# Optimization experiments

Measured on AMD Instinct MI355X. Metric: run time of the kernel, lower is better.

The kernel has to match this reference:

```python
import jax, jax.numpy as jnp
import numpy as np

B, I, H = 16384, 512, 512


def setup_inputs() -> dict:
    key = jax.random.key(0)
    ks = jax.random.split(key, 6)
    scale_s = 1.0 / np.sqrt(H + I + 1)
    scale_g = 1.0 / np.sqrt(H + I + H)
    return {
        "x_t": jax.random.normal(ks[0], (B, I), dtype=jnp.float32),
        "delta_t": jax.random.uniform(ks[1], (B, 1), dtype=jnp.float32),
        "h_prev": jax.random.normal(ks[2], (B, H), dtype=jnp.float32),
        "c_prev": jax.random.normal(ks[3], (B, H), dtype=jnp.float32),
        # linear_s: in = H + I + 1
        "Ws": jax.random.normal(ks[4], (H + I + 1, H), dtype=jnp.float32) * scale_s,
        "bs": jnp.zeros((H,), dtype=jnp.float32),
        # stacked weights for the 5 gates (f, i, T, u, o), each in = H + I + H
        "Wg": jax.random.normal(ks[5], (2 * H + I, 5 * H), dtype=jnp.float32) * scale_g,
        "bg": jnp.zeros((5 * H,), dtype=jnp.float32),
    }


def reference(x_t, delta_t, h_prev, c_prev, Ws, bs, Wg, bg):
    # time gate: s_t = tanh(Linear([h_prev, x_t, delta_t]))
    s_t = jnp.tanh(jnp.concatenate([h_prev, x_t, delta_t], axis=1) @ Ws + bs)
    # shared-input GEMM for the 5 gates on concat([h_prev, x_t, s_t])
    z = jnp.concatenate([h_prev, x_t, s_t], axis=1) @ Wg + bg  # [B, 5H]
    f_t = jax.nn.sigmoid(z[:, 0 * H:1 * H])
    i_t = jax.nn.sigmoid(z[:, 1 * H:2 * H])
    T_t = jax.nn.sigmoid(z[:, 2 * H:3 * H])
    zeta_t = jnp.tanh(z[:, 3 * H:4 * H])
    o_t = jax.nn.sigmoid(z[:, 4 * H:5 * H])
    c_t = f_t * c_prev + i_t * zeta_t + T_t * s_t
    h_t = o_t * jnp.tanh(c_t)
    return (h_t, c_t)
```

## Files before the change

kernel.cpp:

```cpp
#include <hip/hip_runtime.h>
#include <stdint.h>
#include <stddef.h>

#define Bsz 16384
#define Hsz 512
#define KG 1536
#define KA 1024

typedef float f32x4 __attribute__((ext_vector_type(4)));
typedef short bf16x8 __attribute__((ext_vector_type(8)));
typedef unsigned short u16;

__device__ __forceinline__ u16 f2bf(float f) {
  union { float f; unsigned u; } v; v.f = f;
  return (u16)((v.u + 0x7fffu + ((v.u >> 16) & 1u)) >> 16);
}
__device__ __forceinline__ float bf2f(u16 h) {
  union { unsigned u; float f; } v; v.u = ((unsigned)h) << 16;
  return v.f;
}
__device__ __forceinline__ float sigm(float x) {
  return 1.0f / (1.0f + __expf(-x));
}
__device__ __forceinline__ float tanh_(float x) {
  x = fminf(fmaxf(x, -15.0f), 15.0f);
  float e = __expf(2.0f * x);
  return (e - 1.0f) / (e + 1.0f);
}

__device__ __forceinline__ void gload_lds16(const u16* g, u16* l) {
  __builtin_amdgcn_global_load_lds(
      (__attribute__((address_space(1))) void*)(g),
      (__attribute__((address_space(3))) void*)(l), 16, 0, 0);
}

__global__ __launch_bounds__(256) void prep_A_kernel(
    const float* __restrict__ h_prev, const float* __restrict__ x_t,
    u16* __restrict__ A) {
  const int b = blockIdx.x;
  const int q = threadIdx.x;
  const int qq = q & 127;
  const float4* src = (q < 128) ? (const float4*)h_prev : (const float4*)x_t;
  float4 v = src[(size_t)b * 128 + qq];
  ushort4 o;
  o.x = f2bf(v.x); o.y = f2bf(v.y); o.z = f2bf(v.z); o.w = f2bf(v.w);
  *(ushort4*)(A + (size_t)b * KG + (size_t)q * 4) = o;
}

__global__ __launch_bounds__(256) void transpose_cast_kernel(
    const float* __restrict__ in, u16* __restrict__ out, int R, int C) {
  __shared__ float tile[32][33];
  const int c0 = blockIdx.x * 32;
  const int r0 = blockIdx.y * 32;
  const int tx = threadIdx.x;
  const int ty = threadIdx.y;
  #pragma unroll
  for (int i = ty; i < 32; i += 8)
    tile[i][tx] = in[(size_t)(r0 + i) * C + (c0 + tx)];
  __syncthreads();
  #pragma unroll
  for (int i = ty; i < 32; i += 8)
    out[(size_t)(c0 + i) * R + (r0 + tx)] = f2bf(tile[tx][i]);
}

__global__ __launch_bounds__(256, 2) void gemm1_kernel(
    const u16* __restrict__ A, const u16* __restrict__ Wst,
    const float* __restrict__ Ws, const float* __restrict__ bs,
    const float* __restrict__ delta, u16* __restrict__ Aout) {
  __shared__ __attribute__((aligned(16))) u16 Als[128][32];
  __shared__ __attribute__((aligned(16))) u16 Bls[128][32];
  const int t = threadIdx.x;
  const int w = t >> 6, l = t & 63;
  const int bm0 = blockIdx.y * 128;
  const int bn0 = blockIdx.x * 128;
  const int wm = w >> 1, wn = w & 1;

  f32x4 zv = {0.f, 0.f, 0.f, 0.f};
  f32x4 acc[4][4];
  #pragma unroll
  for (int i = 0; i < 4; ++i)
    #pragma unroll
    for (int j = 0; j < 4; ++j) acc[i][j] = zv;

  const int r = t >> 2, q = t & 3;
  const u16* gA0 = A + (size_t)(bm0 + r) * KG + q * 8;
  const u16* gA1 = A + (size_t)(bm0 + 64 + r) * KG + q * 8;
  const u16* gB0 = Wst + (size_t)(bn0 + r) * KA + q * 8;
  const u16* gB1 = Wst + (size_t)(bn0 + 64 + r) * KA + q * 8;
  u16* lA0 = &Als[0][0] + w * 512;
  u16* lA1 = &Als[0][0] + 2048 + w * 512;
  u16* lB0 = &Bls[0][0] + w * 512;
  u16* lB1 = &Bls[0][0] + 2048 + w * 512;

  const int frow = l & 15;
  const int kofs = (l >> 4) * 8;

  for (int kt = 0; kt < KA / 32; ++kt) {
    const int ko = kt * 32;
    gload_lds16(gA0 + ko, lA0);
    gload_lds16(gA1 + ko, lA1);
    gload_lds16(gB0 + ko, lB0);
    gload_lds16(gB1 + ko, lB1);
    __syncthreads();
    bf16x8 af[4], bfv[4];
    #pragma unroll
    for (int mi = 0; mi < 4; ++mi)
      af[mi] = *(const bf16x8*)&Als[wm * 64 + mi * 16 + frow][kofs];
    #pragma unroll
    for (int ni = 0; ni < 4; ++ni)
      bfv[ni] = *(const bf16x8*)&Bls[wn * 64 + ni * 16 + frow][kofs];
    #pragma unroll
    for (int mi = 0; mi < 4; ++mi)
      #pragma unroll
      for (int ni = 0; ni < 4; ++ni)
        acc[mi][ni] = __builtin_amdgcn_mfma_f32_16x16x32_bf16(
            af[mi], bfv[ni], acc[mi][ni], 0, 0, 0);
    __syncthreads();
  }

  #pragma unroll
  for (int ni = 0; ni < 4; ++ni) {
    const int col = bn0 + wn * 64 + ni * 16 + (l & 15);
    const float wsl = Ws[(size_t)1024 * 512 + col];
    const float bsv = bs[col];
    #pragma unroll
    for (int mi = 0; mi < 4; ++mi) {
      #pragma unroll
      for (int rr = 0; rr < 4; ++rr) {
        const int row = bm0 + wm * 64 + mi * 16 + (l >> 4) * 4 + rr;
        const float z = acc[mi][ni][rr] + delta[row] * wsl + bsv;
        Aout[(size_t)row * KG + 1024 + col] = f2bf(tanh_(z));
      }
    }
  }
}

__global__ __launch_bounds__(256, 2) void gemm2_kernel(
    const u16* __restrict__ A, const u16* __restrict__ Wgt,
    const float* __restrict__ bg, const float* __restrict__ c_prev,
    float* __restrict__ out) {
  __shared__ __attribute__((aligned(16))) u16 Als[128][32];
  __shared__ __attribute__((aligned(16))) u16 Bls[160][32];
  const int t = threadIdx.x;
  const int w = t >> 6, l = t & 63;
  const int bm0 = blockIdx.y * 128;
  const int h0 = blockIdx.x * 32;
  const int wm = w >> 1, wh = w & 1;

  f32x4 zv = {0.f, 0.f, 0.f, 0.f};
  f32x4 acc[4][5];
  #pragma unroll
  for (int i = 0; i < 4; ++i)
    #pragma unroll
    for (int j = 0; j < 5; ++j) acc[i][j] = zv;

  const int r = t >> 2, q = t & 3;
  const u16* gA0 = A + (size_t)(bm0 + r) * KG + q * 8;
  const u16* gA1 = A + (size_t)(bm0 + 64 + r) * KG + q * 8;
  const u16* gB0 = Wgt + (size_t)(((r) >> 5) * Hsz + h0 + ((r) & 31)) * KG + q * 8;
  const u16* gB1 = Wgt + (size_t)(((r + 64) >> 5) * Hsz + h0 + ((r + 64) & 31)) * KG + q * 8;
  const u16* gB2 = Wgt + (size_t)(((r + 128) >> 5) * Hsz + h0 + ((r + 128) & 31)) * KG + q * 8;
  u16* lA0 = &Als[0][0] + w * 512;
  u16* lA1 = &Als[0][0] + 2048 + w * 512;
  u16* lB0 = &Bls[0][0] + w * 512;
  u16* lB1 = &Bls[0][0] + 2048 + w * 512;
  u16* lB2 = &Bls[0][0] + 4096 + w * 512;

  const int frow = l & 15;
  const int kofs = (l >> 4) * 8;

  for (int kt = 0; kt < KG / 32; ++kt) {
    const int ko = kt * 32;
    gload_lds16(gA0 + ko, lA0);
    gload_lds16(gA1 + ko, lA1);
    gload_lds16(gB0 + ko, lB0);
    gload_lds16(gB1 + ko, lB1);
    if (t < 128) gload_lds16(gB2 + ko, lB2);
    __syncthreads();
    bf16x8 af[4], bfv[5];
    #pragma unroll
    for (int mi = 0; mi < 4; ++mi)
      af[mi] = *(const bf16x8*)&Als[wm * 64 + mi * 16 + frow][kofs];
    #pragma unroll
    for (int g = 0; g < 5; ++g)
      bfv[g] = *(const bf16x8*)&Bls[g * 32 + wh * 16 + frow][kofs];
    #pragma unroll
    for (int mi = 0; mi < 4; ++mi)
      #pragma unroll
      for (int g = 0; g < 5; ++g)
        acc[mi][g] = __builtin_amdgcn_mfma_f32_16x16x32_bf16(
            af[mi], bfv[g], acc[mi][g], 0, 0, 0);
    __syncthreads();
  }

  const int hc = h0 + wh * 16 + (l & 15);
  const float b_f = bg[hc];
  const float b_i = bg[Hsz + hc];
  const float b_T = bg[2 * Hsz + hc];
  const float b_z = bg[3 * Hsz + hc];
  const float b_o = bg[4 * Hsz + hc];
  #pragma unroll
  for (int mi = 0; mi < 4; ++mi) {
    #pragma unroll
    for (int rr = 0; rr < 4; ++rr) {
      const int row = bm0 + wm * 64 + mi * 16 + (l >> 4) * 4 + rr;
      const float fg = sigm(acc[mi][0][rr] + b_f);
      const float ig = sigm(acc[mi][1][rr] + b_i);
      const float Tg = sigm(acc[mi][2][rr] + b_T);
      const float zg = tanh_(acc[mi][3][rr] + b_z);
      const float og = sigm(acc[mi][4][rr] + b_o);
      const float cp = c_prev[(size_t)row * Hsz + hc];
      const float st = bf2f(A[(size_t)row * KG + 1024 + hc]);
      const float c = fg * cp + ig * zg + Tg * st;
      const float h = og * tanh_(c);
      out[(size_t)row * Hsz + hc] = h;
      out[(size_t)Bsz * Hsz + (size_t)row * Hsz + hc] = c;
    }
  }
}

extern "C" void kernel_launch(void* const* d_in, const int* in_sizes, int n_in,
                              void* d_out, int out_size, void* d_ws, size_t ws_size,
                              hipStream_t stream) {
  const float* x_t    = (const float*)d_in[0];
  const float* delta  = (const float*)d_in[1];
  const float* h_prev = (const float*)d_in[2];
  const float* c_prev = (const float*)d_in[3];
  const float* Ws     = (const float*)d_in[4];
  const float* bs     = (const float*)d_in[5];
  const float* Wg     = (const float*)d_in[6];
  const float* bg     = (const float*)d_in[7];
  float* out = (float*)d_out;

  char* wsb = (char*)d_ws;
  u16* A   = (u16*)(wsb);
  u16* Wst = (u16*)(wsb + (size_t)50331648);
  u16* Wgt = (u16*)(wsb + (size_t)51380224);

  prep_A_kernel<<<dim3(16384), dim3(256), 0, stream>>>(h_prev, x_t, A);
  transpose_cast_kernel<<<dim3(16, 32), dim3(32, 8), 0, stream>>>(Ws, Wst, 1024, 512);
  transpose_cast_kernel<<<dim3(80, 48), dim3(32, 8), 0, stream>>>(Wg, Wgt, 1536, 2560);
  gemm1_kernel<<<dim3(4, 128), dim3(256), 0, stream>>>(A, Wst, Ws, bs, delta, A);
  gemm2_kernel<<<dim3(16, 128), dim3(256), 0, stream>>>(A, Wgt, bg, c_prev, out);
}
```

Before: 220.1 us.

## Rewrite gate GEMM with 4-stage async LDS pipeline, larger tiles and swizzle

The gate GEMM kernel is replaced by a 512-thread version that computes 256x(5*64) tiles. It uses a 4-deep ring of LDS buffers filled by global_load_lds, with explicit vmcnt waits so loads run three K-steps ahead of compute. A XOR swizzle on the LDS layout reduces bank conflicts, and s_setprio is raised around the MFMA block. The aim is to hide global-load latency and improve data reuse. The cost is higher LDS use (about 144KB per block) and more accumulator registers, which may limit occupancy.

```diff
diff --git a/kernel.cpp b/kernel.cpp
--- a/kernel.cpp
+++ b/kernel.cpp
@@ -6,10 +6,12 @@
 #define Hsz 512
 #define KG 1536
 #define KA 1024
+#define NT 48
 
 typedef float f32x4 __attribute__((ext_vector_type(4)));
 typedef short bf16x8 __attribute__((ext_vector_type(8)));
 typedef unsigned short u16;
+typedef unsigned int u32;
 
 __device__ __forceinline__ u16 f2bf(float f) {
   union { float f; unsigned u; } v; v.f = f;
@@ -33,6 +35,8 @@
       (__attribute__((address_space(1))) void*)(g),
       (__attribute__((address_space(3))) void*)(l), 16, 0, 0);
 }
+
+#define VMCNT(n) asm volatile("s_waitcnt vmcnt(" #n ")" ::: "memory")
 
 __global__ __launch_bounds__(256) void prep_A_kernel(
     const float* __restrict__ h_prev, const float* __restrict__ x_t,
@@ -135,75 +139,122 @@
   }
 }
 
-__global__ __launch_bounds__(256, 2) void gemm2_kernel(
+__global__ __launch_bounds__(512, 2) void gemm2_8ph(
     const u16* __restrict__ A, const u16* __restrict__ Wgt,
     const float* __restrict__ bg, const float* __restrict__ c_prev,
     float* __restrict__ out) {
-  __shared__ __attribute__((aligned(16))) u16 Als[128][32];
-  __shared__ __attribute__((aligned(16))) u16 Bls[160][32];
-  const int t = threadIdx.x;
-  const int w = t >> 6, l = t & 63;
-  const int bm0 = blockIdx.y * 128;
-  const int h0 = blockIdx.x * 32;
-  const int wm = w >> 1, wh = w & 1;
+  __shared__ __attribute__((aligned(16))) u16 LDSA[4][256 * 32];
+  __shared__ __attribute__((aligned(16))) u16 LDSB[4][320 * 32];
+
+  const int t5 = threadIdx.x;
+  const int w = t5 >> 6;
+  const int l = t5 & 63;
+
+  const int bid = blockIdx.x;
+  const int hb = bid & 7;
+  const int rb = bid >> 3;
+  const int bm0 = rb * 256;
+  const int h0 = hb * 64;
+
+  const bool isA = (w < 4);
+
+  const u16* gs0 = nullptr; const u16* gs1 = nullptr; const u16* gs2 = nullptr;
+  const u16* gs3 = nullptr; const u16* gs4 = nullptr;
+  u32 lo0 = 0, lo1 = 0, lo2 = 0, lo3 = 0, lo4 = 0;
+
+  if (isA) {
+#define MKA(s, gp, lo) { int idx = w * 256 + (s) * 64 + l; int row = idx >> 2; \
+    int ch = (idx & 3) ^ ((idx >> 3) & 3); \
+    gp = A + (size_t)(bm0 + row) * KG + ch * 8; lo = (u32)(w * 256 + (s) * 64) * 8; }
+    MKA(0, gs0, lo0) MKA(1, gs1, lo1) MKA(2, gs2, lo2) MKA(3, gs3, lo3)
+#undef MKA
+  } else {
+#define MKB(s, gp, lo) { int idx = (w - 4) * 320 + (s) * 64 + l; int rbw = idx >> 2; \
+    int ch = (idx & 3) ^ ((idx >> 3) & 3); \
+    int g = rbw >> 6; int hl = rbw & 63; \
+    gp = Wgt + (size_t)(g * Hsz + h0 + hl) * KG + ch * 8; \
+    lo = (u32)((w - 4) * 320 + (s) * 64) * 8; }
+    MKB(0, gs0, lo0) MKB(1, gs1, lo1) MKB(2, gs2, lo2) MKB(3, gs3, lo3) MKB(4, gs4, lo4)
+#undef MKB
+  }
+
+#define STAGE(kt) { const int _b = (kt) & 3; \
+    if (isA) { \
+      gload_lds16(gs0 + (size_t)(kt) * 32, &LDSA[_b][lo0]); \
+      gload_lds16(gs1 + (size_t)(kt) * 32, &LDSA[_b][lo1]); \
+      gload_lds16(gs2 + (size_t)(kt) * 32, &LDSA[_b][lo2]); \
+      gload_lds16(gs3 + (size_t)(kt) * 32, &LDSA[_b][lo3]); \
+    } else { \
+      gload_lds16(gs0 + (size_t)(kt) * 32, &LDSB[_b][lo0]); \
+      gload_lds16(gs1 + (size_t)(kt) * 32, &LDSB[_b][lo1]); \
+      gload_lds16(gs2 + (size_t)(kt) * 32, &LDSB[_b][lo2]); \
+      gload_lds16(gs3 + (size_t)(kt) * 32, &LDSB[_b][lo3]); \
+      gload_lds16(gs4 + (size_t)(kt) * 32, &LDSB[_b][lo4]); \
+    } }
 
   f32x4 zv = {0.f, 0.f, 0.f, 0.f};
-  f32x4 acc[4][5];
-  #pragma unroll
-  for (int i = 0; i < 4; ++i)
-    #pragma unroll
-    for (int j = 0; j < 5; ++j) acc[i][j] = zv;
-
-  const int r = t >> 2, q = t & 3;
-  const u16* gA0 = A + (size_t)(bm0 + r) * KG + q * 8;
-  const u16* gA1 = A + (size_t)(bm0 + 64 + r) * KG + q * 8;
-  const u16* gB0 = Wgt + (size_t)(((r) >> 5) * Hsz + h0 + ((r) & 31)) * KG + q * 8;
-  const u16* gB1 = Wgt + (size_t)(((r + 64) >> 5) * Hsz + h0 + ((r + 64) & 31)) * KG + q * 8;
-  const u16* gB2 = Wgt + (size_t)(((r + 128) >> 5) * Hsz + h0 + ((r + 128) & 31)) * KG + q * 8;
-  u16* lA0 = &Als[0][0] + w * 512;
-  u16* lA1 = &Als[0][0] + 2048 + w * 512;
-  u16* lB0 = &Bls[0][0] + w * 512;
-  u16* lB1 = &Bls[0][0] + 2048 + w * 512;
-  u16* lB2 = &Bls[0][0] + 4096 + w * 512;
-
+  f32x4 acc[8][5];
+  #pragma unroll
+  for (int mi = 0; mi < 8; ++mi)
+    #pragma unroll
+    for (int g = 0; g < 5; ++g) acc[mi][g] = zv;
+
+  STAGE(0) STAGE(1) STAGE(2)
+
+  const int wm = w >> 2;
+  const int wn = w & 3;
   const int frow = l & 15;
-  const int kofs = (l >> 4) * 8;
-
-  for (int kt = 0; kt < KG / 32; ++kt) {
-    const int ko = kt * 32;
-    gload_lds16(gA0 + ko, lA0);
-    gload_lds16(gA1 + ko, lA1);
-    gload_lds16(gB0 + ko, lB0);
-    gload_lds16(gB1 + ko, lB1);
-    if (t < 128) gload_lds16(gB2 + ko, lB2);
-    __syncthreads();
-    bf16x8 af[4], bfv[5];
-    #pragma unroll
-    for (int mi = 0; mi < 4; ++mi)
-      af[mi] = *(const bf16x8*)&Als[wm * 64 + mi * 16 + frow][kofs];
-    #pragma unroll
-    for (int g = 0; g < 5; ++g)
-      bfv[g] = *(const bf16x8*)&Bls[g * 32 + wh * 16 + frow][kofs];
-    #pragma unroll
-    for (int mi = 0; mi < 4; ++mi)
+  const int kq = l >> 4;
+  const u32 axor = (u32)((kq ^ ((frow >> 1) & 3)) << 3);
+  const u32 abase = (u32)(wm * 128 + frow) * 32 + axor;
+  const u32 bbase = (u32)(wn * 16 + frow) * 32 + axor;
+
+  for (int t = 0; t < NT; ++t) {
+    const int rem = NT - 1 - t;
+    if (rem >= 3) STAGE(t + 3)
+    if (isA) {
+      if (rem >= 3) VMCNT(12); else if (rem == 2) VMCNT(8);
+      else if (rem == 1) VMCNT(4); else VMCNT(0);
+    } else {
+      if (rem >= 3) VMCNT(15); else if (rem == 2) VMCNT(10);
+      else if (rem == 1) VMCNT(5); else VMCNT(0);
+    }
+    __builtin_amdgcn_s_barrier();
+    asm volatile("" ::: "memory");
+
+    const int bt = t & 3;
+    const u16* As = &LDSA[bt][0];
+    const u16* Bs = &LDSB[bt][0];
+    bf16x8 af[8];
+    #pragma unroll
+    for (int mi = 0; mi < 8; ++mi)
+      af[mi] = *(const bf16x8*)&As[abase + mi * 512];
+    __builtin_amdgcn_s_setprio(1);
+    #pragma unroll
+    for (int g = 0; g < 5; ++g) {
+      bf16x8 bf = *(const bf16x8*)&Bs[bbase + g * 2048];
       #pragma unroll
-      for (int g = 0; g < 5; ++g)
+      for (int mi = 0; mi < 8; ++mi)
         acc[mi][g] = __builtin_amdgcn_mfma_f32_16x16x32_bf16(
-            af[mi], bfv[g], acc[mi][g], 0, 0, 0);
-    __syncthreads();
-  }
-
-  const int hc = h0 + wh * 16 + (l & 15);
+            af[mi], bf, acc[mi][g], 0, 0, 0);
+    }
+    __builtin_amdgcn_s_setprio(0);
+    asm volatile("" ::: "memory");
+    __builtin_amdgcn_s_barrier();
+  }
+#undef STAGE
+
+  const int hc = h0 + wn * 16 + frow;
   const float b_f = bg[hc];
   const float b_i = bg[Hsz + hc];
   const float b_T = bg[2 * Hsz + hc];
   const float b_z = bg[3 * Hsz + hc];
   const float b_o = bg[4 * Hsz + hc];
   #pragma unroll
-  for (int mi = 0; mi < 4; ++mi) {
+  for (int mi = 0; mi < 8; ++mi) {
     #pragma unroll
     for (int rr = 0; rr < 4; ++rr) {
-      const int row = bm0 + wm * 64 + mi * 16 + (l >> 4) * 4 + rr;
+      const int row = bm0 + wm * 128 + mi * 16 + kq * 4 + rr;
       const float fg = sigm(acc[mi][0][rr] + b_f);
       const float ig = sigm(acc[mi][1][rr] + b_i);
       const float Tg = sigm(acc[mi][2][rr] + b_T);
@@ -241,5 +292,5 @@
   transpose_cast_kernel<<<dim3(16, 32), dim3(32, 8), 0, stream>>>(Ws, Wst, 1024, 512);
   transpose_cast_kernel<<<dim3(80, 48), dim3(32, 8), 0, stream>>>(Wg, Wgt, 1536, 2560);
   gemm1_kernel<<<dim3(4, 128), dim3(256), 0, stream>>>(A, Wst, Ws, bs, delta, A);
-  gemm2_kernel<<<dim3(16, 128), dim3(256), 0, stream>>>(A, Wgt, bg, c_prev, out);
-}
+  gemm2_8ph<<<dim3(512), dim3(512), 0, stream>>>(A, Wgt, bg, c_prev, out);
+}
```

Result: faster. 209.9 us (-4.6%).

## Double-buffer gemm2 LDS tiles with XOR swizzle and 1D block ordering

Applied to the files above, without the earlier changes.

Rewrites the gate GEMM kernel so the global-to-LDS load of the next K tile is issued while MFMAs run on the current tile, using two LDS buffers and one barrier per iteration instead of two. LDS rows are XOR-swizzled by chunk to cut bank conflicts on the fragment reads. It also uses a 1D grid with h-blocks varying fastest so neighbouring blocks share A rows in cache, raises launch bounds to 3 blocks per CU, and wraps the MFMA block in s_setprio. The cost is double the LDS footprint and extra register pressure, which may limit how many blocks actually fit per CU.

```diff
diff --git a/kernel.cpp b/kernel.cpp
--- a/kernel.cpp
+++ b/kernel.cpp
@@ -6,10 +6,12 @@
 #define Hsz 512
 #define KG 1536
 #define KA 1024
+#define NT3 48
 
 typedef float f32x4 __attribute__((ext_vector_type(4)));
 typedef short bf16x8 __attribute__((ext_vector_type(8)));
 typedef unsigned short u16;
+typedef unsigned int u32;
 
 __device__ __forceinline__ u16 f2bf(float f) {
   union { float f; unsigned u; } v; v.f = f;
@@ -135,65 +137,90 @@
   }
 }
 
-__global__ __launch_bounds__(256, 2) void gemm2_kernel(
+__global__ __launch_bounds__(256, 3) void gemm2_lw(
     const u16* __restrict__ A, const u16* __restrict__ Wgt,
     const float* __restrict__ bg, const float* __restrict__ c_prev,
     float* __restrict__ out) {
-  __shared__ __attribute__((aligned(16))) u16 Als[128][32];
-  __shared__ __attribute__((aligned(16))) u16 Bls[160][32];
-  const int t = threadIdx.x;
-  const int w = t >> 6, l = t & 63;
-  const int bm0 = blockIdx.y * 128;
-  const int h0 = blockIdx.x * 32;
-  const int wm = w >> 1, wh = w & 1;
+  __shared__ __attribute__((aligned(16))) u16 Als[2][128 * 32];
+  __shared__ __attribute__((aligned(16))) u16 Bls[2][160 * 32];
+
+  const int t5 = threadIdx.x;
+  const int w = t5 >> 6;
+  const int l = t5 & 63;
+
+  const int bid = blockIdx.x;
+  const int hb = bid & 15;
+  const int rb = bid >> 4;
+  const int bm0 = rb * 128;
+  const int h0 = hb * 32;
+
+  const u16* gA0; const u16* gA1;
+  const u16* gB0; const u16* gB1; const u16* gB2 = Wgt;
+  u32 loA0, loA1, loB0, loB1, loB2 = 0;
+#define MKA(s, gp, lo) { int idx = (s) * 64 + l; int row = idx >> 2; \
+    int ch = (idx & 3) ^ ((idx >> 3) & 3); \
+    gp = A + (size_t)(bm0 + row) * KG + ch * 8; lo = (u32)(s) * 512; }
+#define MKB(s, gp, lo) { int idx = (s) * 64 + l; int brow = idx >> 2; \
+    int ch = (idx & 3) ^ ((idx >> 3) & 3); \
+    int g = brow >> 5; int hl = brow & 31; \
+    gp = Wgt + (size_t)(g * Hsz + h0 + hl) * KG + ch * 8; lo = (u32)(s) * 512; }
+  MKA(w, gA0, loA0)
+  MKA(w + 4, gA1, loA1)
+  MKB(w, gB0, loB0)
+  MKB(w + 4, gB1, loB1)
+  if (w >= 2) { MKB(w + 6, gB2, loB2) }
+#undef MKA
+#undef MKB
+
+#define STAGE(kt, bb) { \
+    gload_lds16(gA0 + (size_t)(kt) * 32, &Als[bb][loA0]); \
+    gload_lds16(gA1 + (size_t)(kt) * 32, &Als[bb][loA1]); \
+    gload_lds16(gB0 + (size_t)(kt) * 32, &Bls[bb][loB0]); \
+    gload_lds16(gB1 + (size_t)(kt) * 32, &Bls[bb][loB1]); \
+    if (w >= 2) gload_lds16(gB2 + (size_t)(kt) * 32, &Bls[bb][loB2]); \
+  }
 
   f32x4 zv = {0.f, 0.f, 0.f, 0.f};
   f32x4 acc[4][5];
   #pragma unroll
-  for (int i = 0; i < 4; ++i)
-    #pragma unroll
-    for (int j = 0; j < 5; ++j) acc[i][j] = zv;
-
-  const int r = t >> 2, q = t & 3;
-  const u16* gA0 = A + (size_t)(bm0 + r) * KG + q * 8;
-  const u16* gA1 = A + (size_t)(bm0 + 64 + r) * KG + q * 8;
-  const u16* gB0 = Wgt + (size_t)(((r) >> 5) * Hsz + h0 + ((r) & 31)) * KG + q * 8;
-  const u16* gB1 = Wgt + (size_t)(((r + 64) >> 5) * Hsz + h0 + ((r + 64) & 31)) * KG + q * 8;
-  const u16* gB2 = Wgt + (size_t)(((r + 128) >> 5) * Hsz + h0 + ((r + 128) & 31)) * KG + q * 8;
-  u16* lA0 = &Als[0][0] + w * 512;
-  u16* lA1 = &Als[0][0] + 2048 + w * 512;
-  u16* lB0 = &Bls[0][0] + w * 512;
-  u16* lB1 = &Bls[0][0] + 2048 + w * 512;
-  u16* lB2 = &Bls[0][0] + 4096 + w * 512;
-
+  for (int mi = 0; mi < 4; ++mi)
+    #pragma unroll
+    for (int g = 0; g < 5; ++g) acc[mi][g] = zv;
+
+  const int wm = w >> 1;
+  const int wn = w & 1;
   const int frow = l & 15;
-  const int kofs = (l >> 4) * 8;
-
-  for (int kt = 0; kt < KG / 32; ++kt) {
-    const int ko = kt * 32;
-    gload_lds16(gA0 + ko, lA0);
-    gload_lds16(gA1 + ko, lA1);
-    gload_lds16(gB0 + ko, lB0);
-    gload_lds16(gB1 + ko, lB1);
-    if (t < 128) gload_lds16(gB2 + ko, lB2);
-    __syncthreads();
+  const int kq = l >> 4;
+  const u32 axor = (u32)((kq ^ ((frow >> 1) & 3)) << 3);
+
+  STAGE(0, 0)
+  __syncthreads();
+
+  for (int t = 0; t < NT3; ++t) {
+    if (t + 1 < NT3) STAGE(t + 1, (t + 1) & 1)
+    const u16* As = &Als[t & 1][0];
+    const u16* Bs = &Bls[t & 1][0];
     bf16x8 af[4], bfv[5];
     #pragma unroll
     for (int mi = 0; mi < 4; ++mi)
-      af[mi] = *(const bf16x8*)&Als[wm * 64 + mi * 16 + frow][kofs];
+      af[mi] = *(const bf16x8*)&As[(u32)(wm * 64 + mi * 16 + frow) * 32 + axor];
     #pragma unroll
     for (int g = 0; g < 5; ++g)
-      bfv[g] = *(const bf16x8*)&Bls[g * 32 + wh * 16 + frow][kofs];
-    #pragma unroll
-    for (int mi = 0; mi < 4; ++mi)
+      bfv[g] = *(const bf16x8*)&Bs[(u32)(g * 32 + wn * 16 + frow) * 32 + axor];
+    __builtin_amdgcn_s_setprio(1);
+    #pragma unroll
+    for (int g = 0; g < 5; ++g) {
       #pragma unroll
-      for (int g = 0; g < 5; ++g)
+      for (int mi = 0; mi < 4; ++mi)
         acc[mi][g] = __builtin_amdgcn_mfma_f32_16x16x32_bf16(
             af[mi], bfv[g], acc[mi][g], 0, 0, 0);
+    }
+    __builtin_amdgcn_s_setprio(0);
     __syncthreads();
   }
-
-  const int hc = h0 + wh * 16 + (l & 15);
+#undef STAGE
+
+  const int hc = h0 + wn * 16 + frow;
   const float b_f = bg[hc];
   const float b_i = bg[Hsz + hc];
   const float b_T = bg[2 * Hsz + hc];
@@ -203,7 +230,7 @@
   for (int mi = 0; mi < 4; ++mi) {
     #pragma unroll
     for (int rr = 0; rr < 4; ++rr) {
-      const int row = bm0 + wm * 64 + mi * 16 + (l >> 4) * 4 + rr;
+      const int row = bm0 + wm * 64 + mi * 16 + kq * 4 + rr;
       const float fg = sigm(acc[mi][0][rr] + b_f);
       const float ig = sigm(acc[mi][1][rr] + b_i);
       const float Tg = sigm(acc[mi][2][rr] + b_T);
@@ -241,5 +268,5 @@
   transpose_cast_kernel<<<dim3(16, 32), dim3(32, 8), 0, stream>>>(Ws, Wst, 1024, 512);
   transpose_cast_kernel<<<dim3(80, 48), dim3(32, 8), 0, stream>>>(Wg, Wgt, 1536, 2560);
   gemm1_kernel<<<dim3(4, 128), dim3(256), 0, stream>>>(A, Wst, Ws, bs, delta, A);
-  gemm2_kernel<<<dim3(16, 128), dim3(256), 0, stream>>>(A, Wgt, bg, c_prev, out);
-}
+  gemm2_lw<<<dim3(2048), dim3(256), 0, stream>>>(A, Wgt, bg, c_prev, out);
+}
```

After: 222.3 us. No clear change (+1.0%).

## Split gate GEMM into large-tile pipelined MFMA kernel plus separate gate epilogue

Applied to the files above, without the earlier changes.

Replaces the fused gate GEMM (128x160 tiles, single-buffered, sync per k-step) with a 256x256-tile, 512-thread kernel. It double-buffers swizzled LDS tiles, uses inline ds_read_b128, interleaves loads with MFMA quarters, and raises MFMA priority. The GEMM writes z to a bf16 workspace, and a separate gate kernel applies bias, the activations and the cell update with vectorized loads and stores. The goal is more data reuse per tile and latency hiding in the dominant GEMM. The cost is an extra bf16 round trip of z through global memory, plus bf16 rounding of the pre-activations before the gates.

```diff
diff --git a/kernel.cpp b/kernel.cpp
--- a/kernel.cpp
+++ b/kernel.cpp
@@ -6,10 +6,12 @@
 #define Hsz 512
 #define KG 1536
 #define KA 1024
+#define NT2 24
 
 typedef float f32x4 __attribute__((ext_vector_type(4)));
 typedef short bf16x8 __attribute__((ext_vector_type(8)));
 typedef unsigned short u16;
+typedef unsigned int u32;
 
 __device__ __forceinline__ u16 f2bf(float f) {
   union { float f; unsigned u; } v; v.f = f;
@@ -33,6 +35,14 @@
       (__attribute__((address_space(1))) void*)(g),
       (__attribute__((address_space(3))) void*)(l), 16, 0, 0);
 }
+
+#define VMCNT(n) asm volatile("s_waitcnt vmcnt(" #n ")" ::: "memory")
+#define LGKM0() { asm volatile("s_waitcnt lgkmcnt(0)" ::: "memory"); \
+                  __builtin_amdgcn_sched_barrier(0); }
+#define BAR() { asm volatile("" ::: "memory"); __builtin_amdgcn_s_barrier(); \
+                asm volatile("" ::: "memory"); }
+#define DSR(dst, addr, OFF) \
+  asm volatile("ds_read_b128 %0, %1 offset:" #OFF : "=v"(dst) : "v"(addr));
 
 __global__ __launch_bounds__(256) void prep_A_kernel(
     const float* __restrict__ h_prev, const float* __restrict__ x_t,
@@ -135,88 +145,176 @@
   }
 }
 
-__global__ __launch_bounds__(256, 2) void gemm2_kernel(
+__global__ __launch_bounds__(512, 2) void gemm2_t(
     const u16* __restrict__ A, const u16* __restrict__ Wgt,
-    const float* __restrict__ bg, const float* __restrict__ c_prev,
+    u16* __restrict__ z) {
+  __shared__ __attribute__((aligned(16))) u16 LA[2][2][8192];
+  __shared__ __attribute__((aligned(16))) u16 LB[2][2][8192];
+  const int t5 = threadIdx.x;
+  const int w = t5 >> 6, l = t5 & 63;
+  const int bid = blockIdx.x;
+  const int swz = (bid & 7) * 80 + (bid >> 3);
+  const int rb = swz / 10, cb = swz - rb * 10;
+  const int am0 = rb * 256;
+  const int bn0 = cb * 256;
+  const int wm = w >> 2, wn = w & 3;
+
+  const u16 *As00, *As01, *As10, *As11, *Bs00, *Bs01, *Bs10, *Bs11;
+#define MKSRC(P, MAT, BASE, H, J) { \
+    u32 d = (u32)(t5 + (J) * 512) * 16; \
+    u32 row = d >> 7; u32 ch = ((d >> 4) & 7) ^ (row & 7); \
+    P = MAT + (size_t)((BASE) + (H) * 128 + row) * KG + ch * 8; }
+  MKSRC(As00, A, am0, 0, 0) MKSRC(As01, A, am0, 0, 1)
+  MKSRC(As10, A, am0, 1, 0) MKSRC(As11, A, am0, 1, 1)
+  MKSRC(Bs00, Wgt, bn0, 0, 0) MKSRC(Bs01, Wgt, bn0, 0, 1)
+  MKSRC(Bs10, Wgt, bn0, 1, 0) MKSRC(Bs11, Wgt, bn0, 1, 1)
+#undef MKSRC
+
+  const int frow = l & 15, kq = l >> 4;
+  const int f3 = frow & 3, fb2 = (frow >> 2) & 1;
+  const u32 laneC = (u32)((kq ^ f3) * 16);
+  const u32 ldsA0b = (u32)(uintptr_t)&LA[0][0][0];
+  const u32 ldsB0b = (u32)(uintptr_t)&LB[0][0][0];
+  const u32 aAddr0 = ldsA0b + (u32)wm * 16384 + (u32)frow * 128 + (u32)((0 ^ fb2) * 64) + laneC;
+  const u32 aAddr1 = ldsA0b + (u32)wm * 16384 + (u32)frow * 128 + (u32)((1 ^ fb2) * 64) + laneC;
+  const u32 bAddr0 = ldsB0b + (u32)(wn >> 1) * 16384 + (u32)(wn & 1) * 8192 +
+                     (u32)frow * 128 + (u32)((0 ^ fb2) * 64) + laneC;
+  const u32 bAddr1 = ldsB0b + (u32)(wn >> 1) * 16384 + (u32)(wn & 1) * 8192 +
+                     (u32)frow * 128 + (u32)((1 ^ fb2) * 64) + laneC;
+
+  bf16x8 af00, af01, af10, af11, af20, af21, af30, af31;
+  bf16x8 bf00, bf01, bf10, bf11;
+  f32x4 acc[8][4];
+  f32x4 zv = {0.f, 0.f, 0.f, 0.f};
+  #pragma unroll
+  for (int mi = 0; mi < 8; ++mi)
+    #pragma unroll
+    for (int ni = 0; ni < 4; ++ni) acc[mi][ni] = zv;
+
+#define RD_A_B0Q0 { DSR(af00, aAddr0, 0) DSR(af01, aAddr1, 0) \
+    DSR(af10, aAddr0, 2048) DSR(af11, aAddr1, 2048) \
+    DSR(af20, aAddr0, 4096) DSR(af21, aAddr1, 4096) \
+    DSR(af30, aAddr0, 6144) DSR(af31, aAddr1, 6144) }
+#define RD_A_B0Q1 { DSR(af00, aAddr0, 8192) DSR(af01, aAddr1, 8192) \
+    DSR(af10, aAddr0, 10240) DSR(af11, aAddr1, 10240) \
+    DSR(af20, aAddr0, 12288) DSR(af21, aAddr1, 12288) \
+    DSR(af30, aAddr0, 14336) DSR(af31, aAddr1, 14336) }
+#define RD_A_B1Q0 { DSR(af00, aAddr0, 32768) DSR(af01, aAddr1, 32768) \
+    DSR(af10, aAddr0, 34816) DSR(af11, aAddr1, 34816) \
+    DSR(af20, aAddr0, 36864) DSR(af21, aAddr1, 36864) \
+    DSR(af30, aAddr0, 38912) DSR(af31, aAddr1, 38912) }
+#define RD_A_B1Q1 { DSR(af00, aAddr0, 40960) DSR(af01, aAddr1, 40960) \
+    DSR(af10, aAddr0, 43008) DSR(af11, aAddr1, 43008) \
+    DSR(af20, aAddr0, 45056) DSR(af21, aAddr1, 45056) \
+    DSR(af30, aAddr0, 47104) DSR(af31, aAddr1, 47104) }
+#define RD_B_B0Q0 { DSR(bf00, bAddr0, 0) DSR(bf01, bAddr1, 0) \
+    DSR(bf10, bAddr0, 2048) DSR(bf11, bAddr1, 2048) }
+#define RD_B_B0Q1 { DSR(bf00, bAddr0, 4096) DSR(bf01, bAddr1, 4096) \
+    DSR(bf10, bAddr0, 6144) DSR(bf11, bAddr1, 6144) }
+#define RD_B_B1Q0 { DSR(bf00, bAddr0, 32768) DSR(bf01, bAddr1, 32768) \
+    DSR(bf10, bAddr0, 34816) DSR(bf11, bAddr1, 34816) }
+#define RD_B_B1Q1 { DSR(bf00, bAddr0, 36864) DSR(bf01, bAddr1, 36864) \
+    DSR(bf10, bAddr0, 38912) DSR(bf11, bAddr1, 38912) }
+
+#define MM(FI, KS, NI, QM, QN) \
+  acc[(QM)*4+(FI)][(QN)*2+(NI)] = __builtin_amdgcn_mfma_f32_16x16x32_bf16( \
+      af##FI##KS, bf##NI##KS, acc[(QM)*4+(FI)][(QN)*2+(NI)], 0, 0, 0);
+#define MFMA16(QM, QN) { __builtin_amdgcn_s_setprio(1); \
+    MM(0,0,0,QM,QN) MM(1,0,0,QM,QN) MM(2,0,0,QM,QN) MM(3,0,0,QM,QN) \
+    MM(0,0,1,QM,QN) MM(1,0,1,QM,QN) MM(2,0,1,QM,QN) MM(3,0,1,QM,QN) \
+    MM(0,1,0,QM,QN) MM(1,1,0,QM,QN) MM(2,1,0,QM,QN) MM(3,1,0,QM,QN) \
+    MM(0,1,1,QM,QN) MM(1,1,1,QM,QN) MM(2,1,1,QM,QN) MM(3,1,1,QM,QN) \
+    __builtin_amdgcn_s_setprio(0); }
+
+#define STG_AH0(tl, NB) { gload_lds16(As00 + (size_t)(tl) * 64, &LA[NB][0][0] + t5 * 8); \
+                          gload_lds16(As01 + (size_t)(tl) * 64, &LA[NB][0][0] + t5 * 8 + 4096); }
+#define STG_AH1(tl, NB) { gload_lds16(As10 + (size_t)(tl) * 64, &LA[NB][1][0] + t5 * 8); \
+                          gload_lds16(As11 + (size_t)(tl) * 64, &LA[NB][1][0] + t5 * 8 + 4096); }
+#define STG_BH0(tl, NB) { gload_lds16(Bs00 + (size_t)(tl) * 64, &LB[NB][0][0] + t5 * 8); \
+                          gload_lds16(Bs01 + (size_t)(tl) * 64, &LB[NB][0][0] + t5 * 8 + 4096); }
+#define STG_BH1(tl, NB) { gload_lds16(Bs10 + (size_t)(tl) * 64, &LB[NB][1][0] + t5 * 8); \
+                          gload_lds16(Bs11 + (size_t)(tl) * 64, &LB[NB][1][0] + t5 * 8 + 4096); }
+
+#define GROUP(RDA0, RDA1, RDB0, RDB1, NB, j) { \
+    const int tl = (j) + 1; const bool st = (j) < NT2 - 1; \
+    RDA0 RDB0 \
+    if (st) STG_AH0(tl, NB) \
+    BAR(); LGKM0(); MFMA16(0, 0) BAR(); \
+    RDB1 \
+    if (st) STG_AH1(tl, NB) \
+    BAR(); LGKM0(); MFMA16(0, 1) BAR(); \
+    RDA1 \
+    if (st) STG_BH0(tl, NB) \
+    BAR(); LGKM0(); MFMA16(1, 1) BAR(); \
+    RDB0 \
+    if (st) STG_BH1(tl, NB) \
+    BAR(); LGKM0(); MFMA16(1, 0) \
+    VMCNT(0); BAR(); }
+
+  STG_AH0(0, 0) STG_AH1(0, 0) STG_BH0(0, 0) STG_BH1(0, 0)
+  VMCNT(0);
+  BAR();
+
+  for (int j2 = 0; j2 < NT2; j2 += 2) {
+    GROUP(RD_A_B0Q0, RD_A_B0Q1, RD_B_B0Q0, RD_B_B0Q1, 1, j2)
+    GROUP(RD_A_B1Q0, RD_A_B1Q1, RD_B_B1Q0, RD_B_B1Q1, 0, j2 + 1)
+  }
+
+  #pragma unroll
+  for (int mi = 0; mi < 8; ++mi) {
+    #pragma unroll
+    for (int ni = 0; ni < 4; ++ni) {
+      #pragma unroll
+      for (int rr = 0; rr < 4; ++rr) {
+        const int row = am0 + wm * 128 + mi * 16 + kq * 4 + rr;
+        const int col = bn0 + wn * 64 + ni * 16 + frow;
+        z[(size_t)row * 2560 + col] = f2bf(acc[mi][ni][rr]);
+      }
+    }
+  }
+}
+
+__global__ __launch_bounds__(256) void gate_kernel(
+    const u16* __restrict__ z, const u16* __restrict__ A,
+    const float* __restrict__ c_prev, const float* __restrict__ bg,
     float* __restrict__ out) {
-  __shared__ __attribute__((aligned(16))) u16 Als[128][32];
-  __shared__ __attribute__((aligned(16))) u16 Bls[160][32];
   const int t = threadIdx.x;
-  const int w = t >> 6, l = t & 63;
-  const int bm0 = blockIdx.y * 128;
-  const int h0 = blockIdx.x * 32;
-  const int wm = w >> 1, wh = w & 1;
-
-  f32x4 zv = {0.f, 0.f, 0.f, 0.f};
-  f32x4 acc[4][5];
-  #pragma unroll
-  for (int i = 0; i < 4; ++i)
-    #pragma unroll
-    for (int j = 0; j < 5; ++j) acc[i][j] = zv;
-
-  const int r = t >> 2, q = t & 3;
-  const u16* gA0 = A + (size_t)(bm0 + r) * KG + q * 8;
-  const u16* gA1 = A + (size_t)(bm0 + 64 + r) * KG + q * 8;
-  const u16* gB0 = Wgt + (size_t)(((r) >> 5) * Hsz + h0 + ((r) & 31)) * KG + q * 8;
-  const u16* gB1 = Wgt + (size_t)(((r + 64) >> 5) * Hsz + h0 + ((r + 64) & 31)) * KG + q * 8;
-  const u16* gB2 = Wgt + (size_t)(((r + 128) >> 5) * Hsz + h0 + ((r + 128) & 31)) * KG + q * 8;
-  u16* lA0 = &Als[0][0] + w * 512;
-  u16* lA1 = &Als[0][0] + 2048 + w * 512;
-  u16* lB0 = &Bls[0][0] + w * 512;
-  u16* lB1 = &Bls[0][0] + 2048 + w * 512;
-  u16* lB2 = &Bls[0][0] + 4096 + w * 512;
-
-  const int frow = l & 15;
-  const int kofs = (l >> 4) * 8;
-
-  for (int kt = 0; kt < KG / 32; ++kt) {
-    const int ko = kt * 32;
-    gload_lds16(gA0 + ko, lA0);
-    gload_lds16(gA1 + ko, lA1);
-    gload_lds16(gB0 + ko, lB0);
-    gload_lds16(gB1 + ko, lB1);
-    if (t < 128) gload_lds16(gB2 + ko, lB2);
-    __syncthreads();
-    bf16x8 af[4], bfv[5];
-    #pragma unroll
-    for (int mi = 0; mi < 4; ++mi)
-      af[mi] = *(const bf16x8*)&Als[wm * 64 + mi * 16 + frow][kofs];
-    #pragma unroll
-    for (int g = 0; g < 5; ++g)
-      bfv[g] = *(const bf16x8*)&Bls[g * 32 + wh * 16 + frow][kofs];
-    #pragma unroll
-    for (int mi = 0; mi < 4; ++mi)
-      #pragma unroll
-      for (int g = 0; g < 5; ++g)
-        acc[mi][g] = __builtin_amdgcn_mfma_f32_16x16x32_bf16(
-            af[mi], bfv[g], acc[mi][g], 0, 0, 0);
-    __syncthreads();
-  }
-
-  const int hc = h0 + wh * 16 + (l & 15);
-  const float b_f = bg[hc];
-  const float b_i = bg[Hsz + hc];
-  const float b_T = bg[2 * Hsz + hc];
-  const float b_z = bg[3 * Hsz + hc];
-  const float b_o = bg[4 * Hsz + hc];
-  #pragma unroll
-  for (int mi = 0; mi < 4; ++mi) {
-    #pragma unroll
-    for (int rr = 0; rr < 4; ++rr) {
-      const int row = bm0 + wm * 64 + mi * 16 + (l >> 4) * 4 + rr;
-      const float fg = sigm(acc[mi][0][rr] + b_f);
-      const float ig = sigm(acc[mi][1][rr] + b_i);
-      const float Tg = sigm(acc[mi][2][rr] + b_T);
-      const float zg = tanh_(acc[mi][3][rr] + b_z);
-      const float og = sigm(acc[mi][4][rr] + b_o);
-      const float cp = c_prev[(size_t)row * Hsz + hc];
-      const float st = bf2f(A[(size_t)row * KG + 1024 + hc]);
-      const float c = fg * cp + ig * zg + Tg * st;
-      const float h = og * tanh_(c);
-      out[(size_t)row * Hsz + hc] = h;
-      out[(size_t)Bsz * Hsz + (size_t)row * Hsz + hc] = c;
-    }
-  }
+  const int r = blockIdx.x * 4 + (t >> 6);
+  const int h0 = (t & 63) * 8;
+  const u16* zr = z + (size_t)r * 2560;
+
+  float zg[5][8];
+  #pragma unroll
+  for (int g = 0; g < 5; ++g) {
+    bf16x8 v = *(const bf16x8*)(zr + g * 512 + h0);
+    #pragma unroll
+    for (int j = 0; j < 8; ++j)
+      zg[g][j] = bf2f((u16)v[j]) + bg[g * 512 + h0 + j];
+  }
+  bf16x8 sv = *(const bf16x8*)(A + (size_t)r * KG + 1024 + h0);
+  float4 cp0 = *(const float4*)(c_prev + (size_t)r * 512 + h0);
+  float4 cp1 = *(const float4*)(c_prev + (size_t)r * 512 + h0 + 4);
+
+  float hv[8], cv[8];
+  #pragma unroll
+  for (int j = 0; j < 8; ++j) {
+    const float cp = (j < 4) ? ((const float*)&cp0)[j] : ((const float*)&cp1)[j - 4];
+    const float fg = sigm(zg[0][j]);
+    const float ig = sigm(zg[1][j]);
+    const float Tg = sigm(zg[2][j]);
+    const float ze = tanh_(zg[3][j]);
+    const float og = sigm(zg[4][j]);
+    const float st = bf2f((u16)sv[j]);
+    const float c = fg * cp + ig * ze + Tg * st;
+    hv[j] = og * tanh_(c);
+    cv[j] = c;
+  }
+  float* oh = out + (size_t)r * 512 + h0;
+  float* oc = out + (size_t)Bsz * Hsz + (size_t)r * 512 + h0;
+  *(float4*)(oh) = make_float4(hv[0], hv[1], hv[2], hv[3]);
+  *(float4*)(oh + 4) = make_float4(hv[4], hv[5], hv[6], hv[7]);
+  *(float4*)(oc) = make_float4(cv[0], cv[1], cv[2], cv[3]);
+  *(float4*)(oc + 4) = make_float4(cv[4], cv[5], cv[6], cv[7]);
 }
 
 extern "C" void kernel_launch(void* const* d_in, const int* in_sizes, int n_in,
@@ -236,10 +334,12 @@
   u16* A   = (u16*)(wsb);
   u16* Wst = (u16*)(wsb + (size_t)50331648);
   u16* Wgt = (u16*)(wsb + (size_t)51380224);
+  u16* zbuf = (u16*)(wsb + (size_t)59244544);
 
   prep_A_kernel<<<dim3(16384), dim3(256), 0, stream>>>(h_prev, x_t, A);
   transpose_cast_kernel<<<dim3(16, 32), dim3(32, 8), 0, stream>>>(Ws, Wst, 1024, 512);
   transpose_cast_kernel<<<dim3(80, 48), dim3(32, 8), 0, stream>>>(Wg, Wgt, 1536, 2560);
   gemm1_kernel<<<dim3(4, 128), dim3(256), 0, stream>>>(A, Wst, Ws, bs, delta, A);
-  gemm2_kernel<<<dim3(16, 128), dim3(256), 0, stream>>>(A, Wgt, bg, c_prev, out);
-}
+  gemm2_t<<<dim3(640), dim3(512), 0, stream>>>(A, Wgt, zbuf);
+  gate_kernel<<<dim3(4096), dim3(256), 0, stream>>>(zbuf, A, c_prev, bg, out);
+}
```

Result: slower. 240.7 us (+9.4%).
